# Optimization experiments

Hardware: AMD Instinct MI355X
Metric: run time of the kernel (lower is better)

## Reference

```python
import jax, jax.numpy as jnp
import numpy as np

SEQ, BATCH, HID = 2048, 4, 1024


def setup_inputs() -> dict:
    key = jax.random.key(0)
    ks = jax.random.split(key, 8)
    s = 1.0 / np.sqrt(HID)
    return {
        "x": jax.random.normal(ks[0], (SEQ, BATCH, HID), dtype=jnp.float32),
        "ssm": jax.random.uniform(ks[1], (BATCH, SEQ, SEQ), dtype=jnp.float32),
        "Wq": jax.random.uniform(ks[2], (HID, HID), jnp.float32, -s, s),
        "bq": jax.random.uniform(ks[3], (HID,), jnp.float32, -s, s),
        "Wk": jax.random.uniform(ks[4], (HID, HID), jnp.float32, -s, s),
        "bk": jax.random.uniform(ks[5], (HID,), jnp.float32, -s, s),
        "Wv": jax.random.uniform(ks[6], (HID, HID), jnp.float32, -s, s),
        "bv": jax.random.uniform(ks[7], (HID,), jnp.float32, -s, s),
    }


def reference(x, ssm, Wq, bq, Wk, bk, Wv, bv):
    # x: [seq, batch, hid]; torch Linear: y = x @ W.T + b
    scale = jnp.asarray(HID ** 0.5, x.dtype)
    Q = x @ Wq.T + bq                      # [s, b, h]
    K = x @ Wk.T + bk
    V = x @ Wv.T + bv
    # transpose to batch-first: [b, s, h]
    Q = jnp.transpose(Q, (1, 0, 2))
    K = jnp.transpose(K, (1, 0, 2))
    V = jnp.transpose(V, (1, 0, 2))
    scores = jnp.einsum('bqh,bkh->bqk', Q, K) / scale   # [b, s, s]
    masked = scores * ssm                                # multiplicative mask on raw scores
    attn = jax.nn.softmax(masked, axis=-1)
    out = jnp.einsum('bqk,bkh->bqh', attn, V)            # [b, s, h]
    return jnp.transpose(out, (1, 0, 2))                 # [s, b, h]
```

## Files before the change

### kernel.cpp

```cpp
#include <hip/hip_runtime.h>
#include <hip/hip_bf16.h>

#define SEQ 2048
#define BATCH 4
#define HID 1024

typedef __bf16 bf16x8 __attribute__((ext_vector_type(8)));
typedef __bf16 bf16x4 __attribute__((ext_vector_type(4)));
typedef float f32x4 __attribute__((ext_vector_type(4)));

__device__ __forceinline__ void gload_lds16(void* lds, const void* g) {
  __builtin_amdgcn_global_load_lds(
      (const __attribute__((address_space(1))) void*)g,
      (__attribute__((address_space(3))) void*)lds, 16, 0, 0);
}

__global__ __launch_bounds__(256) void cast_f32_bf16(const float* __restrict__ in,
                                                     __bf16* __restrict__ out, int n8) {
  int i = blockIdx.x * 256 + threadIdx.x;
  if (i >= n8) return;
  const float4* p = (const float4*)in + (size_t)i * 2;
  float4 a = p[0], b = p[1];
  bf16x8 v;
  v[0] = (__bf16)a.x; v[1] = (__bf16)a.y; v[2] = (__bf16)a.z; v[3] = (__bf16)a.w;
  v[4] = (__bf16)b.x; v[5] = (__bf16)b.y; v[6] = (__bf16)b.z; v[7] = (__bf16)b.w;
  ((bf16x8*)out)[i] = v;
}

__global__ __launch_bounds__(256) void cast_w3(const float* __restrict__ w0,
                                               const float* __restrict__ w1,
                                               const float* __restrict__ w2,
                                               __bf16* __restrict__ out) {
  const int wsel = blockIdx.y;
  const float* src = wsel == 0 ? w0 : wsel == 1 ? w1 : w2;
  int i = blockIdx.x * 256 + threadIdx.x;
  const float4* p = (const float4*)src + (size_t)i * 2;
  float4 a = p[0], b = p[1];
  bf16x8 v;
  v[0] = (__bf16)a.x; v[1] = (__bf16)a.y; v[2] = (__bf16)a.z; v[3] = (__bf16)a.w;
  v[4] = (__bf16)b.x; v[5] = (__bf16)b.y; v[6] = (__bf16)b.z; v[7] = (__bf16)b.w;
  ((bf16x8*)(out + (size_t)wsel * HID * HID))[i] = v;
}

__global__ void concat_bias(const float* b0, const float* b1, const float* b2,
                            float* __restrict__ out) {
  const float* s = blockIdx.x == 0 ? b0 : blockIdx.x == 1 ? b1 : b2;
  out[blockIdx.x * HID + threadIdx.x] = s[threadIdx.x];
}

#define SLOT 49152
template<int EPI>
__global__ __launch_bounds__(512, 2)
void gemm8(const __bf16* __restrict__ A, int lda, long long sAz,
           const __bf16* __restrict__ B, int ldb, long long sBz,
           const float* __restrict__ aux, void* __restrict__ dst,
           float* __restrict__ aux2, int K)
{
  __shared__ __align__(16) char lds[3 * SLOT];
  const int tid = threadIdx.x;
  const int wid = tid >> 6, lane = tid & 63;
  const int wr = wid >> 2, wc = wid & 3;
  const int m0 = blockIdx.x * 128, n0 = blockIdx.y * 256;
  const int z = blockIdx.z;
  const __bf16* Ab = A + (size_t)z * sAz;
  const __bf16* Bb = B + (size_t)z * sBz;

  const int srow = tid >> 3;
  const int scol = ((tid & 7) * 16) ^ ((srow & 7) << 4);
  const char* asrc0 = (const char*)(Ab + (size_t)(m0 + srow) * lda) + scol;
  const char* asrc1 = (const char*)(Ab + (size_t)(m0 + srow + 64) * lda) + scol;
  const char* bsrc0 = (const char*)(Bb + (size_t)(n0 + srow) * ldb) + scol;
  const char* bsrc1 = (const char*)(Bb + (size_t)(n0 + srow + 64) * ldb) + scol;
  const char* bsrc2 = (const char*)(Bb + (size_t)(n0 + srow + 128) * ldb) + scol;
  const char* bsrc3 = (const char*)(Bb + (size_t)(n0 + srow + 192) * ldb) + scol;
  const int dA = tid * 16, dB = 16384 + tid * 16;

  const int fr = lane & 15, fq = lane >> 4;
  const int fc2 = fq * 16;
  const int swz = (fr & 7) << 4;
  int aoff[4][2], boff[4][2];
#pragma unroll
  for (int mi = 0; mi < 4; ++mi) {
    const int row = wr * 64 + mi * 16 + fr;
#pragma unroll
    for (int ks = 0; ks < 2; ++ks)
      aoff[mi][ks] = row * 128 + ((fc2 + ks * 64) ^ swz);
  }
#pragma unroll
  for (int ni = 0; ni < 4; ++ni) {
    const int row = wc * 64 + ni * 16 + fr;
#pragma unroll
    for (int ks = 0; ks < 2; ++ks)
      boff[ni][ks] = 16384 + row * 128 + ((fc2 + ks * 64) ^ swz);
  }

  const int nk = K >> 6;
  {
    char* s0 = lds;
    gload_lds16(s0 + dA, asrc0); gload_lds16(s0 + dA + 8192, asrc1);
    gload_lds16(s0 + dB, bsrc0); gload_lds16(s0 + dB + 8192, bsrc1);
    gload_lds16(s0 + dB + 16384, bsrc2); gload_lds16(s0 + dB + 24576, bsrc3);
    char* s1 = lds + SLOT;
    gload_lds16(s1 + dA, asrc0 + 128); gload_lds16(s1 + dA + 8192, asrc1 + 128);
    gload_lds16(s1 + dB, bsrc0 + 128); gload_lds16(s1 + dB + 8192, bsrc1 + 128);
    gload_lds16(s1 + dB + 16384, bsrc2 + 128); gload_lds16(s1 + dB + 24576, bsrc3 + 128);
  }

  f32x4 acc[4][4] = {};
  for (int t = 0; t < nk; ++t) {
    char* s = lds + (t % 3) * SLOT;
    if (t + 1 < nk) asm volatile("s_waitcnt vmcnt(6)" ::: "memory");
    else            asm volatile("s_waitcnt vmcnt(0)" ::: "memory");
    __builtin_amdgcn_s_barrier();
    asm volatile("" ::: "memory");

    bf16x8 a[4][2], b[4][2];
#pragma unroll
    for (int mi = 0; mi < 4; ++mi)
#pragma unroll
      for (int ks = 0; ks < 2; ++ks)
        a[mi][ks] = *(const bf16x8*)(s + aoff[mi][ks]);
#pragma unroll
    for (int ni = 0; ni < 4; ++ni)
#pragma unroll
      for (int ks = 0; ks < 2; ++ks)
        b[ni][ks] = *(const bf16x8*)(s + boff[ni][ks]);

    if (t + 2 < nk) {
      char* sn = lds + ((t + 2) % 3) * SLOT;
      const size_t ko = (size_t)(t + 2) * 128;
      gload_lds16(sn + dA, asrc0 + ko);
      gload_lds16(sn + dA + 8192, asrc1 + ko);
      gload_lds16(sn + dB, bsrc0 + ko);
      gload_lds16(sn + dB + 8192, bsrc1 + ko);
      gload_lds16(sn + dB + 16384, bsrc2 + ko);
      gload_lds16(sn + dB + 24576, bsrc3 + ko);
    }

    __builtin_amdgcn_s_setprio(1);
#pragma unroll
    for (int mi = 0; mi < 4; ++mi)
#pragma unroll
      for (int ni = 0; ni < 4; ++ni)
#pragma unroll
        for (int ks = 0; ks < 2; ++ks)
          acc[mi][ni] = __builtin_amdgcn_mfma_f32_16x16x32_bf16(a[mi][ks], b[ni][ks], acc[mi][ni], 0, 0, 0);
    __builtin_amdgcn_s_setprio(0);
  }
  __syncthreads();

  if (EPI == 0) {
    const int hsel = n0 >> 10;
    const size_t BSH = (size_t)BATCH * SEQ * HID;
#pragma unroll
    for (int mi = 0; mi < 4; ++mi) {
#pragma unroll
      for (int ni = 0; ni < 4; ++ni) {
        const int gn = n0 + wc * 64 + ni * 16 + fr;
        const int h = gn & (HID - 1);
        const int gmb = m0 + wr * 64 + mi * 16 + fq * 4;
        const float bias = aux[gn];
        f32x4 v = acc[mi][ni];
        if (hsel < 2) {
#pragma unroll
          for (int r = 0; r < 4; ++r)
            ((__bf16*)dst)[(size_t)hsel * BSH + (size_t)z * SEQ * HID +
                           (size_t)(gmb + r) * HID + h] = (__bf16)(v[r] + bias);
        } else {
          bf16x4 vv;
#pragma unroll
          for (int r = 0; r < 4; ++r) vv[r] = (__bf16)(v[r] + bias);
          *(bf16x4*)&((__bf16*)dst)[2 * BSH + (size_t)z * HID * SEQ +
                                    (size_t)h * SEQ + gmb] = vv;
        }
      }
    }
  } else if (EPI == 2) {
    float psum[4][4] = {};
#pragma unroll
    for (int mi = 0; mi < 4; ++mi) {
#pragma unroll
      for (int ni = 0; ni < 4; ++ni) {
        const int gn = n0 + wc * 64 + ni * 16 + fr;
        const int gmb = m0 + wr * 64 + mi * 16 + fq * 4;
        f32x4 v = acc[mi][ni];
#pragma unroll
        for (int r = 0; r < 4; ++r) {
          const size_t idx = (size_t)z * SEQ * SEQ + (size_t)(gmb + r) * SEQ + gn;
          const float e = __expf(v[r] * 0.03125f * aux[idx]);
          ((__bf16*)dst)[idx] = (__bf16)e;
          psum[mi][r] += e;
        }
      }
    }
#pragma unroll
    for (int mi = 0; mi < 4; ++mi)
#pragma unroll
      for (int r = 0; r < 4; ++r) {
        float sv = psum[mi][r];
        sv += __shfl_xor(sv, 1); sv += __shfl_xor(sv, 2);
        sv += __shfl_xor(sv, 4); sv += __shfl_xor(sv, 8);
        psum[mi][r] = sv;
      }
    float* red = (float*)lds;
    if (fr == 0) {
#pragma unroll
      for (int mi = 0; mi < 4; ++mi)
#pragma unroll
        for (int r = 0; r < 4; ++r)
          red[wid * 64 + mi * 16 + fq * 4 + r] = psum[mi][r];
    }
    __syncthreads();
    if (tid < 128) {
      const int half = tid >> 6, r64 = tid & 63;
      float sv = 0.f;
#pragma unroll
      for (int j = 0; j < 4; ++j) sv += red[(half * 4 + j) * 64 + r64];
      aux2[((size_t)z * SEQ + m0 + tid) * 8 + blockIdx.y] = sv;
    }
  } else {
    float* red = (float*)lds;
    if (tid < 128) {
      const float* pp = aux + ((size_t)z * SEQ + m0 + tid) * 8;
      float sv = 0.f;
#pragma unroll
      for (int j = 0; j < 8; ++j) sv += pp[j];
      red[tid] = 1.f / sv;
    }
    __syncthreads();
#pragma unroll
    for (int mi = 0; mi < 4; ++mi) {
#pragma unroll
      for (int ni = 0; ni < 4; ++ni) {
        const int gn = n0 + wc * 64 + ni * 16 + fr;
        const int rbase = wr * 64 + mi * 16 + fq * 4;
        f32x4 v = acc[mi][ni];
#pragma unroll
        for (int r = 0; r < 4; ++r)
          ((float*)dst)[((size_t)(m0 + rbase + r) * BATCH + z) * HID + gn] = v[r] * red[rbase + r];
      }
    }
  }
}

extern "C" void kernel_launch(void* const* d_in, const int* in_sizes, int n_in,
                              void* d_out, int out_size, void* d_ws, size_t ws_size,
                              hipStream_t stream) {
  const float* x   = (const float*)d_in[0];
  const float* ssm = (const float*)d_in[1];
  const float* Wq  = (const float*)d_in[2];
  const float* bq  = (const float*)d_in[3];
  const float* Wk  = (const float*)d_in[4];
  const float* bk  = (const float*)d_in[5];
  const float* Wv  = (const float*)d_in[6];
  const float* bv  = (const float*)d_in[7];
  float* out = (float*)d_out;

  const size_t BSH = (size_t)BATCH * SEQ * HID;
  float* bqkv    = (float*)d_ws;
  float* partial = bqkv + 4096;
  __bf16* xbf  = (__bf16*)(partial + (size_t)BATCH * SEQ * 8);
  __bf16* wqkv = xbf + BSH;
  __bf16* Qb = wqkv + (size_t)3 * HID * HID;
  __bf16* Kb = Qb + BSH;
  __bf16* Vt = Qb + 2 * BSH;
  __bf16* E  = Qb + 3 * BSH;

  cast_f32_bf16<<<(int)(BSH / 8 / 256), 256, 0, stream>>>(x, xbf, (int)(BSH / 8));
  cast_w3<<<dim3(HID * HID / 8 / 256, 3), 256, 0, stream>>>(Wq, Wk, Wv, wqkv);
  concat_bias<<<3, HID, 0, stream>>>(bq, bk, bv, bqkv);

  gemm8<0><<<dim3(16, 12, BATCH), 512, 0, stream>>>(xbf, BATCH * HID, HID,
                                                    wqkv, HID, 0, bqkv, Qb, nullptr, HID);
  gemm8<2><<<dim3(16, 8, BATCH), 512, 0, stream>>>(Qb, HID, (long long)SEQ * HID,
                                                   Kb, HID, (long long)SEQ * HID,
                                                   ssm, E, partial, HID);
  gemm8<3><<<dim3(16, 4, BATCH), 512, 0, stream>>>(E, SEQ, (long long)SEQ * SEQ,
                                                   Vt, SEQ, (long long)HID * SEQ,
                                                   partial, out, nullptr, SEQ);
}
```

Measured before the change: 155.6 us.

## Merge prep casts into one kernel and remap GEMM tiles across XCDs

Replaces the three preprocessing launches (x cast, weight casts, bias concat) with a single prep kernel, removing two launch gaps. In the GEMM, linear block IDs are remapped so that consecutive hardware-dispatched blocks (round-robined over 8 XCDs) get contiguous tiles, aiming for better L2 reuse of shared A/B panels per XCD. The remap assumes the x*y tile count is divisible by 8, which holds for the grids used.

```diff
diff --git a/kernel.cpp b/kernel.cpp
--- a/kernel.cpp
+++ b/kernel.cpp
@@ -15,10 +15,8 @@
       (__attribute__((address_space(3))) void*)lds, 16, 0, 0);
 }
 
-__global__ __launch_bounds__(256) void cast_f32_bf16(const float* __restrict__ in,
-                                                     __bf16* __restrict__ out, int n8) {
-  int i = blockIdx.x * 256 + threadIdx.x;
-  if (i >= n8) return;
+__device__ __forceinline__ void cast8(const float* __restrict__ in,
+                                      __bf16* __restrict__ out, int i) {
   const float4* p = (const float4*)in + (size_t)i * 2;
   float4 a = p[0], b = p[1];
   bf16x8 v;
@@ -27,25 +25,31 @@
   ((bf16x8*)out)[i] = v;
 }
 
-__global__ __launch_bounds__(256) void cast_w3(const float* __restrict__ w0,
-                                               const float* __restrict__ w1,
-                                               const float* __restrict__ w2,
-                                               __bf16* __restrict__ out) {
-  const int wsel = blockIdx.y;
-  const float* src = wsel == 0 ? w0 : wsel == 1 ? w1 : w2;
-  int i = blockIdx.x * 256 + threadIdx.x;
-  const float4* p = (const float4*)src + (size_t)i * 2;
-  float4 a = p[0], b = p[1];
-  bf16x8 v;
-  v[0] = (__bf16)a.x; v[1] = (__bf16)a.y; v[2] = (__bf16)a.z; v[3] = (__bf16)a.w;
-  v[4] = (__bf16)b.x; v[5] = (__bf16)b.y; v[6] = (__bf16)b.z; v[7] = (__bf16)b.w;
-  ((bf16x8*)(out + (size_t)wsel * HID * HID))[i] = v;
-}
-
-__global__ void concat_bias(const float* b0, const float* b1, const float* b2,
-                            float* __restrict__ out) {
-  const float* s = blockIdx.x == 0 ? b0 : blockIdx.x == 1 ? b1 : b2;
-  out[blockIdx.x * HID + threadIdx.x] = s[threadIdx.x];
+#define NX (SEQ * BATCH * HID / 8)
+#define NWI (HID * HID / 8)
+
+__global__ __launch_bounds__(256) void prep(const float* __restrict__ x,
+                                            const float* __restrict__ Wq,
+                                            const float* __restrict__ Wk,
+                                            const float* __restrict__ Wv,
+                                            const float* __restrict__ bq,
+                                            const float* __restrict__ bk,
+                                            const float* __restrict__ bv,
+                                            __bf16* __restrict__ xbf,
+                                            __bf16* __restrict__ wqkv,
+                                            float* __restrict__ bqkv) {
+  int id = blockIdx.x * 256 + threadIdx.x;
+  if (id < NX) {
+    cast8(x, xbf, id);
+  } else if (id < NX + 3 * NWI) {
+    const int j = id - NX;
+    const int w = j / NWI, k = j - w * NWI;
+    const float* src = w == 0 ? Wq : w == 1 ? Wk : Wv;
+    cast8(src, wqkv + (size_t)w * HID * HID, k);
+  } else if (id < NX + 3 * NWI + 3 * HID) {
+    const int j = id - (NX + 3 * NWI);
+    bqkv[j] = j < HID ? bq[j] : j < 2 * HID ? bk[j - HID] : bv[j - 2 * HID];
+  }
 }
 
 #define SLOT 49152
@@ -60,7 +64,13 @@
   const int tid = threadIdx.x;
   const int wid = tid >> 6, lane = tid & 63;
   const int wr = wid >> 2, wc = wid & 3;
-  const int m0 = blockIdx.x * 128, n0 = blockIdx.y * 256;
+
+  const int nx = gridDim.x, nxy = nx * gridDim.y;
+  const int f = blockIdx.x + nx * blockIdx.y;
+  const int tile = (f & 7) * (nxy >> 3) + (f >> 3);
+  const int bx = tile % nx, by = tile / nx;
+
+  const int m0 = bx * 128, n0 = by * 256;
   const int z = blockIdx.z;
   const __bf16* Ab = A + (size_t)z * sAz;
   const __bf16* Bb = B + (size_t)z * sBz;
@@ -216,7 +226,7 @@
       float sv = 0.f;
 #pragma unroll
       for (int j = 0; j < 4; ++j) sv += red[(half * 4 + j) * 64 + r64];
-      aux2[((size_t)z * SEQ + m0 + tid) * 8 + blockIdx.y] = sv;
+      aux2[((size_t)z * SEQ + m0 + tid) * 8 + by] = sv;
     }
   } else {
     float* red = (float*)lds;
@@ -266,9 +276,9 @@
   __bf16* Vt = Qb + 2 * BSH;
   __bf16* E  = Qb + 3 * BSH;
 
-  cast_f32_bf16<<<(int)(BSH / 8 / 256), 256, 0, stream>>>(x, xbf, (int)(BSH / 8));
-  cast_w3<<<dim3(HID * HID / 8 / 256, 3), 256, 0, stream>>>(Wq, Wk, Wv, wqkv);
-  concat_bias<<<3, HID, 0, stream>>>(bq, bk, bv, bqkv);
+  const int prep_items = NX + 3 * NWI + 3 * HID;
+  prep<<<(prep_items + 255) / 256, 256, 0, stream>>>(x, Wq, Wk, Wv, bq, bk, bv,
+                                                     xbf, wqkv, bqkv);
 
   gemm8<0><<<dim3(16, 12, BATCH), 512, 0, stream>>>(xbf, BATCH * HID, HID,
                                                     wqkv, HID, 0, bqkv, Qb, nullptr, HID);
```

New measurement: 163.5 us. +5.1%, slower.
